# Performance work log

Hardware: AMD Instinct MI355X
Metric: run time of the kernel (lower is better)

## Reference

```python
import jax, jax.numpy as jnp
import numpy as np

B, S, E, H, L, F, V = 8, 1024, 768, 12, 6, 3072, 32000
HD = E // H  # head_dim = 64
EPS = 1e-5


def _pos_encoding(max_len, dim):
    pos = np.arange(max_len, dtype=np.float32)[:, None]
    div = np.exp(np.arange(0, dim, 2, dtype=np.float32) * (-np.log(10000.0) / dim))
    pe = np.zeros((max_len, dim), dtype=np.float32)
    pe[:, 0::2] = np.sin(pos * div)
    pe[:, 1::2] = np.cos(pos * div)
    return jnp.asarray(pe)


def setup_inputs() -> dict:
    key = jax.random.key(0)
    ks = jax.random.split(key, 16)
    sd = 0.02
    inp = {}
    inp['input_ids'] = jax.random.randint(ks[0], (B, S), 0, V)
    inp['attention_mask'] = jnp.ones((B, S), dtype=jnp.int32)
    inp['emb'] = jax.random.normal(ks[1], (V, E), jnp.float32) * sd
    inp['pe'] = _pos_encoding(S, E)
    inp['Wq'] = jax.random.normal(ks[2], (L, E, E), jnp.float32) * sd
    inp['bq'] = jnp.zeros((L, E), jnp.float32)
    inp['Wk'] = jax.random.normal(ks[3], (L, E, E), jnp.float32) * sd
    inp['bk'] = jnp.zeros((L, E), jnp.float32)
    inp['Wv'] = jax.random.normal(ks[4], (L, E, E), jnp.float32) * sd
    inp['bv'] = jnp.zeros((L, E), jnp.float32)
    inp['Wo'] = jax.random.normal(ks[5], (L, E, E), jnp.float32) * sd
    inp['bo'] = jnp.zeros((L, E), jnp.float32)
    inp['ln1_g'] = jnp.ones((L, E), jnp.float32)
    inp['ln1_b'] = jnp.zeros((L, E), jnp.float32)
    inp['W1'] = jax.random.normal(ks[6], (L, E, F), jnp.float32) * sd
    inp['b1'] = jnp.zeros((L, F), jnp.float32)
    inp['W2'] = jax.random.normal(ks[7], (L, F, E), jnp.float32) * sd
    inp['b2'] = jnp.zeros((L, E), jnp.float32)
    inp['ln2_g'] = jnp.ones((L, E), jnp.float32)
    inp['ln2_b'] = jnp.zeros((L, E), jnp.float32)
    inp['Wc'] = jax.random.normal(ks[8], (E, 2), jnp.float32) * sd
    inp['bc'] = jnp.zeros((2,), jnp.float32)
    return inp


def _layernorm(x, g, b):
    mu = jnp.mean(x, axis=-1, keepdims=True)
    var = jnp.mean(jnp.square(x - mu), axis=-1, keepdims=True)
    return (x - mu) * jax.lax.rsqrt(var + EPS) * g + b


def reference(input_ids, attention_mask, emb, pe, Wq, bq, Wk, bk, Wv, bv, Wo, bo,
              ln1_g, ln1_b, W1, b1, W2, b2, ln2_g, ln2_b, Wc, bc):
    x = emb[input_ids] + pe[None, :S, :]           # [B,S,E] (dropout = eval identity)
    mask = attention_mask[:, None, None, :]        # [B,1,1,S]
    scale = jnp.sqrt(jnp.float32(HD))

    def block(x, p):
        wq, bq_, wk, bk_, wv, bv_, wo, bo_, g1, be1, w1, b1_, w2, b2_, g2, be2 = p
        q = (x @ wq + bq_).reshape(B, S, H, HD).transpose(0, 2, 1, 3)  # [B,H,S,D]
        k = (x @ wk + bk_).reshape(B, S, H, HD).transpose(0, 2, 1, 3)
        v = (x @ wv + bv_).reshape(B, S, H, HD).transpose(0, 2, 1, 3)
        scores = jnp.einsum('bhsd,bhtd->bhst', q, k) / scale          # [B,H,S,S]
        scores = jnp.where(mask == 0, -jnp.inf, scores)
        attn = jax.nn.softmax(scores, axis=-1)
        o = jnp.einsum('bhst,bhtd->bhsd', attn, v)
        o = o.transpose(0, 2, 1, 3).reshape(B, S, E) @ wo + bo_
        x = _layernorm(x + o, g1, be1)
        ffn = jax.nn.relu(x @ w1 + b1_) @ w2 + b2_
        x = _layernorm(x + ffn, g2, be2)
        return x, None

    params = (Wq, bq, Wk, bk, Wv, bv, Wo, bo, ln1_g, ln1_b, W1, b1, W2, b2, ln2_g, ln2_b)
    x, _ = jax.lax.scan(block, x, params)
    pooled = jnp.mean(x, axis=1)                   # [B,E]
    return pooled @ Wc + bc                        # [B,2]
```

## Files before the change

kernel.cpp:

```cpp
#include <hip/hip_runtime.h>

typedef __bf16 bf16x8 __attribute__((ext_vector_type(8)));
typedef float  f32x4  __attribute__((ext_vector_type(4)));

constexpr int Bb = 8, Ss = 1024, Ee = 768, Hh = 12, Ll = 6, Ff = 3072;
constexpr int TOK  = Bb * Ss;
constexpr int NQKV = 3 * Ee;

static __device__ __forceinline__ f32x4 mfma16(bf16x8 a, bf16x8 b, f32x4 c) {
  return __builtin_amdgcn_mfma_f32_16x16x32_bf16(a, b, c, 0, 0, 0);
}

static __device__ __forceinline__ void async16(const void* g, void* l) {
  __builtin_amdgcn_global_load_lds(
      (const __attribute__((address_space(1))) unsigned int*)g,
      (__attribute__((address_space(3))) unsigned int*)l, 16, 0, 0);
}

static __device__ __forceinline__ bf16x8 ds_read128(const __bf16* p) {
  bf16x8 r;
  unsigned a = (unsigned)(size_t)p;
  asm volatile("ds_read_b128 %0, %1" : "=v"(r) : "v"(a));
  return r;
}

__global__ __launch_bounds__(256) void embed_kernel(
    const int* __restrict__ ids, const float* __restrict__ emb,
    const float* __restrict__ pe, float* __restrict__ x, __bf16* __restrict__ xb)
{
  int tok = blockIdx.x;
  int s   = tok & (Ss - 1);
  int id  = ids[tok];
  const float* er = emb + (size_t)id * Ee;
  const float* pr = pe  + (size_t)s  * Ee;
  size_t base = (size_t)tok * Ee;
#pragma unroll
  for (int i = 0; i < 3; i++) {
    int e = threadIdx.x + i * 256;
    float v = er[e] + pr[e];
    x[base + e]  = v;
    xb[base + e] = (__bf16)v;
  }
}

__global__ __launch_bounds__(256) void transpose_w_kernel(
    const float* __restrict__ src, __bf16* __restrict__ dst,
    int K, int N, size_t sls, size_t dls)
{
  __shared__ float t[32][33];
  src += (size_t)blockIdx.z * sls;
  dst += (size_t)blockIdx.z * dls;
  int n0 = blockIdx.x * 32, k0 = blockIdx.y * 32;
  int c = threadIdx.x & 31, r0 = threadIdx.x >> 5;
#pragma unroll
  for (int rr = 0; rr < 32; rr += 8)
    t[r0 + rr][c] = src[(size_t)(k0 + r0 + rr) * N + n0 + c];
  __syncthreads();
#pragma unroll
  for (int rr = 0; rr < 32; rr += 8)
    dst[(size_t)(n0 + r0 + rr) * K + k0 + c] = (__bf16)t[c][r0 + rr];
}

template<bool OUT_BF16, bool RELU>
__global__ __launch_bounds__(256, 3) void gemm_kernel(
    const __bf16* __restrict__ A, const __bf16* __restrict__ Bt,
    const float* __restrict__ bias0, const float* __restrict__ bias1,
    const float* __restrict__ bias2, int bseg,
    float* __restrict__ Cf, __bf16* __restrict__ Cb, int M, int N, int K)
{
  __shared__ __align__(16) __bf16 lA[3][64 * 64];
  __shared__ __align__(16) __bf16 lB[3][64 * 64];
  const int tid  = threadIdx.x;
  const int wave = tid >> 6, lane = tid & 63;
  const int quad = lane >> 4, c16 = lane & 15;
  const int wm = wave >> 1, wn = wave & 1;

  const int bid = blockIdx.x;
  const int xcd = bid & 7;
  const int lb  = bid >> 3;
  const int mb  = xcd * 8 + (lb & 7);
  const int nb  = lb >> 3;
  const size_t m0 = (size_t)mb * 128, n0 = (size_t)nb * 128;

  f32x4 acc[4][4] = {};

  const int s0l = tid >> 3;
  const int s0c = tid & 7;
  const int l0  = s0c ^ (s0l & 7);
  const int tr0 = (s0l << 1) | (l0 >> 2);
  const int gc0 = (l0 & 3) * 8;
  const int s1l = (tid + 256) >> 3;
  const int l1  = s0c ^ (s1l & 7);
  const int tr1 = (s1l << 1) | (l1 >> 2);
  const int gc1 = (l1 & 3) * 8;

  const __bf16* Ag0 = A  + (m0 + tr0) * K + gc0;
  const __bf16* Ag1 = A  + (m0 + tr1) * K + gc1;
  const __bf16* Bg0 = Bt + (n0 + tr0) * K + gc0;
  const __bf16* Bg1 = Bt + (n0 + tr1) * K + gc1;
  const int d0 = tid * 8;

  const int nk = K >> 5;

  auto stage = [&](int t, int slot) {
    const int kof = t << 5;
    async16(Ag0 + kof, &lA[slot][d0]);
    async16(Ag1 + kof, &lA[slot][d0 + 2048]);
    async16(Bg0 + kof, &lB[slot][d0]);
    async16(Bg1 + kof, &lB[slot][d0 + 2048]);
  };

  int aoff[4], boff[4];
#pragma unroll
  for (int f = 0; f < 4; f++) {
    int ra = wm * 64 + f * 16 + c16;
    int ja = ra >> 1;
    aoff[f] = ja * 64 + (((((ra & 1) << 2) | quad)) ^ (ja & 7)) * 8;
    int rb = wn * 64 + f * 16 + c16;
    int jb = rb >> 1;
    boff[f] = jb * 64 + (((((rb & 1) << 2) | quad)) ^ (jb & 7)) * 8;
  }

  stage(0, 0);
  stage(1, 1);
  asm volatile("s_waitcnt vmcnt(4)" ::: "memory");
  __builtin_amdgcn_s_barrier();
  __builtin_amdgcn_sched_barrier(0);

  int slot = 0;
  for (int t = 0; t < nk; ++t) {
    if (t + 2 < nk) {
      int ns = slot + 2; if (ns >= 3) ns -= 3;
      stage(t + 2, ns);
    }
    const __bf16* la = &lA[slot][0];
    const __bf16* lb = &lB[slot][0];
    bf16x8 af[4], bfr[4];
#pragma unroll
    for (int f = 0; f < 4; f++) af[f]  = ds_read128(la + aoff[f]);
#pragma unroll
    for (int f = 0; f < 4; f++) bfr[f] = ds_read128(lb + boff[f]);
    asm volatile("s_waitcnt lgkmcnt(0)" ::: "memory");
    __builtin_amdgcn_sched_barrier(0);
    __builtin_amdgcn_s_setprio(1);
#pragma unroll
    for (int mi = 0; mi < 4; mi++)
#pragma unroll
      for (int ni = 0; ni < 4; ni++)
        acc[mi][ni] = mfma16(af[mi], bfr[ni], acc[mi][ni]);
    __builtin_amdgcn_s_setprio(0);
    __builtin_amdgcn_sched_barrier(0);
    if (t + 2 < nk) asm volatile("s_waitcnt vmcnt(4)" ::: "memory");
    else            asm volatile("s_waitcnt vmcnt(0)" ::: "memory");
    __builtin_amdgcn_s_barrier();
    __builtin_amdgcn_sched_barrier(0);
    slot = (slot + 1 == 3) ? 0 : slot + 1;
  }

#pragma unroll
  for (int ni = 0; ni < 4; ni++) {
    int col = (int)n0 + wn * 64 + ni * 16 + c16;
    const float* bp = bias0;
    int cc = col;
    if (cc >= bseg) { bp = bias1; cc -= bseg; }
    if (cc >= bseg) { bp = bias2; cc -= bseg; }
    float bv = bp[cc];
#pragma unroll
    for (int mi = 0; mi < 4; mi++) {
#pragma unroll
      for (int rr = 0; rr < 4; rr++) {
        size_t row = m0 + wm * 64 + mi * 16 + quad * 4 + rr;
        float v = acc[mi][ni][rr] + bv;
        if (RELU) v = fmaxf(v, 0.f);
        if (OUT_BF16) Cb[row * N + col] = (__bf16)v;
        else          Cf[row * N + col] = v;
      }
    }
  }
}

__global__ __launch_bounds__(256) void vtrans_kernel(
    const __bf16* __restrict__ qkv, __bf16* __restrict__ vt)
{
  int tid  = blockIdx.x * 256 + threadIdx.x;
  int d    = tid & 63;
  int rest = tid >> 6;
  int sc   = rest & 127;
  int bh   = rest >> 7;
  int b = bh / Hh, h = bh % Hh;
  const __bf16* src = qkv + (size_t)(b * Ss + sc * 8) * NQKV + 2 * Ee + h * 64 + d;
  bf16x8 v;
#pragma unroll
  for (int i = 0; i < 8; i++) v[i] = src[(size_t)i * NQKV];
  *(bf16x8*)(vt + ((size_t)bh * 64 + d) * Ss + sc * 8) = v;
}

__global__ __launch_bounds__(512, 6) void attn_kernel(
    const __bf16* __restrict__ qkv, const __bf16* __restrict__ vt,
    const int* __restrict__ amask, __bf16* __restrict__ out)
{
  __shared__ __align__(16) __bf16 kbuf[2][64 * 64];
  __shared__ __align__(16) __bf16 vbuf[2][64 * 64];
  __shared__ __align__(16) __bf16 plds[8][16 * 68];
  const int idx = blockIdx.x;
  const int bh = idx % 96, qi = idx / 96;
  const int b = bh / Hh, h = bh % Hh;
  const int lane = threadIdx.x & 63, wave = threadIdx.x >> 6;
  const int quad = lane >> 4, c16 = lane & 15;
  const int q0 = qi * 128 + wave * 16;

  const __bf16* qbase = qkv + (size_t)(b * Ss + q0 + c16) * NQKV + h * 64 + quad * 8;
  bf16x8 qf0 = *(const bf16x8*)(qbase);
  bf16x8 qf1 = *(const bf16x8*)(qbase + 32);

  const int srow = threadIdx.x >> 3;
  const int scol = ((threadIdx.x & 7) ^ (srow & 7)) * 8;
  const __bf16* kg = qkv + (size_t)(b * Ss + srow) * NQKV + Ee + h * 64 + scol;
  const __bf16* vg = vt + ((size_t)bh * 64 + srow) * Ss + scol;

  const int sa8 = c16 & 7;
  const int rc0 = (quad ^ sa8) * 8;
  const int rc1 = ((quad + 4) ^ sa8) * 8;

  f32x4 o[4] = {};
  float lrow[4] = {0.f, 0.f, 0.f, 0.f};
  const int* mp = amask + b * Ss;
  __bf16* pw = &plds[wave][0];

  async16(kg, &kbuf[0][(size_t)threadIdx.x * 8]);
  async16(vg, &vbuf[0][(size_t)threadIdx.x * 8]);

  for (int t = 0; t < 16; t++) {
    const int tb = t * 64;
    __syncthreads();
    if (t < 15) {
      const int nb = (t + 1) & 1, ntb = tb + 64;
      async16(kg + (size_t)ntb * NQKV, &kbuf[nb][(size_t)threadIdx.x * 8]);
      async16(vg + ntb,                &vbuf[nb][(size_t)threadIdx.x * 8]);
    }
    const __bf16* kb = &kbuf[t & 1][0];
    const __bf16* vb = &vbuf[t & 1][0];

    f32x4 s[4];
#pragma unroll
    for (int n = 0; n < 4; n++) {
      bf16x8 kf0 = *(const bf16x8*)(kb + (n * 16 + c16) * 64 + rc0);
      bf16x8 kf1 = *(const bf16x8*)(kb + (n * 16 + c16) * 64 + rc1);
      f32x4 z = {};
      z = mfma16(qf0, kf0, z);
      s[n] = mfma16(qf1, kf1, z);
    }
    float mk[4];
#pragma unroll
    for (int n = 0; n < 4; n++) mk[n] = mp[tb + n * 16 + c16] ? 0.f : -1e30f;

#pragma unroll
    for (int rr = 0; rr < 4; rr++) {
      float p0 = __expf(s[0][rr] * 0.125f + mk[0]);
      float p1 = __expf(s[1][rr] * 0.125f + mk[1]);
      float p2 = __expf(s[2][rr] * 0.125f + mk[2]);
      float p3 = __expf(s[3][rr] * 0.125f + mk[3]);
      lrow[rr] += (p0 + p1) + (p2 + p3);
      int prow = (quad * 4 + rr) * 68;
      pw[prow + 0  + c16] = (__bf16)p0;
      pw[prow + 16 + c16] = (__bf16)p1;
      pw[prow + 32 + c16] = (__bf16)p2;
      pw[prow + 48 + c16] = (__bf16)p3;
    }

    bf16x8 pf0 = *(const bf16x8*)(pw + c16 * 68 + quad * 8);
    bf16x8 pf1 = *(const bf16x8*)(pw + c16 * 68 + 32 + quad * 8);
#pragma unroll
    for (int ni = 0; ni < 4; ni++) {
      bf16x8 vf0 = *(const bf16x8*)(vb + (ni * 16 + c16) * 64 + rc0);
      bf16x8 vf1 = *(const bf16x8*)(vb + (ni * 16 + c16) * 64 + rc1);
      o[ni] = mfma16(pf0, vf0, o[ni]);
      o[ni] = mfma16(pf1, vf1, o[ni]);
    }
  }

#pragma unroll
  for (int rr = 0; rr < 4; rr++) {
    float sr = lrow[rr];
    sr += __shfl_xor(sr, 1);
    sr += __shfl_xor(sr, 2);
    sr += __shfl_xor(sr, 4);
    sr += __shfl_xor(sr, 8);
    float inv = 1.f / sr;
    size_t row = (size_t)(b * Ss + q0 + quad * 4 + rr) * Ee + h * 64;
    out[row + 0  + c16] = (__bf16)(o[0][rr] * inv);
    out[row + 16 + c16] = (__bf16)(o[1][rr] * inv);
    out[row + 32 + c16] = (__bf16)(o[2][rr] * inv);
    out[row + 48 + c16] = (__bf16)(o[3][rr] * inv);
  }
}

__global__ __launch_bounds__(256) void add_ln_kernel(
    const float* __restrict__ xin, const float* __restrict__ tmp,
    const float* __restrict__ g, const float* __restrict__ beta,
    float* __restrict__ xout, __bf16* __restrict__ xbout)
{
  __shared__ float red[8];
  size_t base = (size_t)blockIdx.x * Ee;
  float hv[3], s = 0.f, sq = 0.f;
#pragma unroll
  for (int i = 0; i < 3; i++) {
    int e = threadIdx.x + i * 256;
    hv[i] = xin[base + e] + tmp[base + e];
    s += hv[i]; sq += hv[i] * hv[i];
  }
#pragma unroll
  for (int m = 1; m < 64; m <<= 1) { s += __shfl_xor(s, m); sq += __shfl_xor(sq, m); }
  int wave = threadIdx.x >> 6;
  if ((threadIdx.x & 63) == 0) { red[wave] = s; red[4 + wave] = sq; }
  __syncthreads();
  s  = red[0] + red[1] + red[2] + red[3];
  sq = red[4] + red[5] + red[6] + red[7];
  float mean = s * (1.f / Ee);
  float var  = sq * (1.f / Ee) - mean * mean;
  float rstd = rsqrtf(var + 1e-5f);
#pragma unroll
  for (int i = 0; i < 3; i++) {
    int e = threadIdx.x + i * 256;
    float v = (hv[i] - mean) * rstd * g[e] + beta[e];
    xout[base + e]  = v;
    xbout[base + e] = (__bf16)v;
  }
}

__global__ __launch_bounds__(256) void pool1_kernel(
    const float* __restrict__ x, float* __restrict__ partial)
{
  int b = blockIdx.x, chunk = blockIdx.y;
  float acc[3] = {0.f, 0.f, 0.f};
  for (int s = chunk * 64; s < chunk * 64 + 64; s++) {
#pragma unroll
    for (int i = 0; i < 3; i++) {
      int e = threadIdx.x + i * 256;
      acc[i] += x[((size_t)b * Ss + s) * Ee + e];
    }
  }
#pragma unroll
  for (int i = 0; i < 3; i++) {
    int e = threadIdx.x + i * 256;
    partial[((size_t)b * 16 + chunk) * Ee + e] = acc[i];
  }
}

__global__ __launch_bounds__(256) void pool2_kernel(
    const float* __restrict__ partial, const float* __restrict__ Wc,
    const float* __restrict__ bc, float* __restrict__ out)
{
  __shared__ float red[8];
  int b = blockIdx.x;
  float p0 = 0.f, p1 = 0.f;
#pragma unroll
  for (int i = 0; i < 3; i++) {
    int e = threadIdx.x + i * 256;
    float pe_ = 0.f;
#pragma unroll
    for (int c = 0; c < 16; c++) pe_ += partial[((size_t)b * 16 + c) * Ee + e];
    pe_ *= (1.f / Ss);
    p0 += pe_ * Wc[e * 2 + 0];
    p1 += pe_ * Wc[e * 2 + 1];
  }
#pragma unroll
  for (int m = 1; m < 64; m <<= 1) { p0 += __shfl_xor(p0, m); p1 += __shfl_xor(p1, m); }
  int wave = threadIdx.x >> 6;
  if ((threadIdx.x & 63) == 0) { red[wave] = p0; red[4 + wave] = p1; }
  __syncthreads();
  if (threadIdx.x == 0) {
    out[b * 2 + 0] = red[0] + red[1] + red[2] + red[3] + bc[0];
    out[b * 2 + 1] = red[4] + red[5] + red[6] + red[7] + bc[1];
  }
}

extern "C" void kernel_launch(void* const* d_in, const int* in_sizes, int n_in,
                              void* d_out, int out_size, void* d_ws, size_t ws_size,
                              hipStream_t stream) {
  const int*   ids   = (const int*)  d_in[0];
  const int*   amask = (const int*)  d_in[1];
  const float* emb   = (const float*)d_in[2];
  const float* pe    = (const float*)d_in[3];
  const float* Wq    = (const float*)d_in[4];
  const float* bq    = (const float*)d_in[5];
  const float* Wk    = (const float*)d_in[6];
  const float* bk    = (const float*)d_in[7];
  const float* Wv    = (const float*)d_in[8];
  const float* bv    = (const float*)d_in[9];
  const float* Wo    = (const float*)d_in[10];
  const float* bo    = (const float*)d_in[11];
  const float* ln1g  = (const float*)d_in[12];
  const float* ln1b  = (const float*)d_in[13];
  const float* W1    = (const float*)d_in[14];
  const float* b1    = (const float*)d_in[15];
  const float* W2    = (const float*)d_in[16];
  const float* b2    = (const float*)d_in[17];
  const float* ln2g  = (const float*)d_in[18];
  const float* ln2b  = (const float*)d_in[19];
  const float* Wc    = (const float*)d_in[20];
  const float* bc    = (const float*)d_in[21];
  float* outp = (float*)d_out;

  char* p = (char*)d_ws;
  auto alloc = [&](size_t bytes) { char* r = p; p += (bytes + 255) & ~(size_t)255; return r; };
  float*  x     = (float*) alloc((size_t)TOK * Ee * 4);
  __bf16* xb    = (__bf16*)alloc((size_t)TOK * Ee * 2);
  float*  tmp   = (float*) alloc((size_t)TOK * Ee * 4);
  __bf16* attn  = (__bf16*)alloc((size_t)TOK * Ee * 2);
  char*   r1    = alloc((size_t)TOK * Ff * 2);
  __bf16* qkv   = (__bf16*)r1;
  __bf16* vt    = (__bf16*)(r1 + (size_t)TOK * NQKV * 2);
  __bf16* h1    = (__bf16*)r1;
  __bf16* wqkvt = (__bf16*)alloc((size_t)Ll * NQKV * Ee * 2);
  __bf16* wot   = (__bf16*)alloc((size_t)Ll * Ee * Ee * 2);
  __bf16* w1t   = (__bf16*)alloc((size_t)Ll * Ff * Ee * 2);
  __bf16* w2t   = (__bf16*)alloc((size_t)Ll * Ee * Ff * 2);
  float*  part  = (float*) alloc((size_t)Bb * 16 * Ee * 4);

  embed_kernel<<<TOK, 256, 0, stream>>>(ids, emb, pe, x, xb);

  transpose_w_kernel<<<dim3(Ee/32, Ee/32, Ll), 256, 0, stream>>>(
      Wq, wqkvt,                         Ee, Ee, (size_t)Ee*Ee, (size_t)NQKV*Ee);
  transpose_w_kernel<<<dim3(Ee/32, Ee/32, Ll), 256, 0, stream>>>(
      Wk, wqkvt + (size_t)Ee*Ee,         Ee, Ee, (size_t)Ee*Ee, (size_t)NQKV*Ee);
  transpose_w_kernel<<<dim3(Ee/32, Ee/32, Ll), 256, 0, stream>>>(
      Wv, wqkvt + (size_t)2*Ee*Ee,       Ee, Ee, (size_t)Ee*Ee, (size_t)NQKV*Ee);
  transpose_w_kernel<<<dim3(Ee/32, Ee/32, Ll), 256, 0, stream>>>(
      Wo, wot,                           Ee, Ee, (size_t)Ee*Ee, (size_t)Ee*Ee);
  transpose_w_kernel<<<dim3(Ff/32, Ee/32, Ll), 256, 0, stream>>>(
      W1, w1t,                           Ee, Ff, (size_t)Ee*Ff, (size_t)Ff*Ee);
  transpose_w_kernel<<<dim3(Ee/32, Ff/32, Ll), 256, 0, stream>>>(
      W2, w2t,                           Ff, Ee, (size_t)Ff*Ee, (size_t)Ee*Ff);

  for (int l = 0; l < Ll; l++) {
    gemm_kernel<true, false><<<64 * (NQKV/128), 256, 0, stream>>>(
        xb, wqkvt + (size_t)l*NQKV*Ee,
        bq + l*Ee, bk + l*Ee, bv + l*Ee, Ee,
        nullptr, qkv, TOK, NQKV, Ee);
    vtrans_kernel<<<3072, 256, 0, stream>>>(qkv, vt);
    attn_kernel<<<768, 512, 0, stream>>>(qkv, vt, amask, attn);
    gemm_kernel<false, false><<<64 * (Ee/128), 256, 0, stream>>>(
        attn, wot + (size_t)l*Ee*Ee,
        bo + l*Ee, bo + l*Ee, bo + l*Ee, Ee,
        tmp, nullptr, TOK, Ee, Ee);
    add_ln_kernel<<<TOK, 256, 0, stream>>>(x, tmp, ln1g + l*Ee, ln1b + l*Ee, x, xb);
    gemm_kernel<true, true><<<64 * (Ff/128), 256, 0, stream>>>(
        xb, w1t + (size_t)l*Ff*Ee,
        b1 + l*Ff, b1 + l*Ff, b1 + l*Ff, Ff,
        nullptr, h1, TOK, Ff, Ee);
    gemm_kernel<false, false><<<64 * (Ee/128), 256, 0, stream>>>(
        h1, w2t + (size_t)l*Ee*Ff,
        b2 + l*Ee, b2 + l*Ee, b2 + l*Ee, Ee,
        tmp, nullptr, TOK, Ee, Ff);
    add_ln_kernel<<<TOK, 256, 0, stream>>>(x, tmp, ln2g + l*Ee, ln2b + l*Ee, x, xb);
  }

  pool1_kernel<<<dim3(Bb, 16), 256, 0, stream>>>(x, part);
  pool2_kernel<<<Bb, 256, 0, stream>>>(part, Wc, bc, outp);
}
```

Baseline: 1.910 ms.

## Add 256x128 triple-buffered GEMM for QKV/FFN1 and use exp2 in attention

```diff
diff --git a/kernel.cpp b/kernel.cpp
--- a/kernel.cpp
+++ b/kernel.cpp
@@ -22,6 +22,10 @@
   unsigned a = (unsigned)(size_t)p;
   asm volatile("ds_read_b128 %0, %1" : "=v"(r) : "v"(a));
   return r;
+}
+
+static __device__ __forceinline__ float fexp2(float x) {
+  float r; asm("v_exp_f32 %0, %1" : "=v"(r) : "v"(x)); return r;
 }
 
 __global__ __launch_bounds__(256) void embed_kernel(
@@ -179,6 +183,130 @@
   }
 }
 
+template<bool RELU>
+__global__ __launch_bounds__(256, 2) void gemm_big_kernel(
+    const __bf16* __restrict__ A, const __bf16* __restrict__ Bt,
+    const float* __restrict__ bias0, const float* __restrict__ bias1,
+    const float* __restrict__ bias2, int bseg,
+    __bf16* __restrict__ Cb, int N, int K)
+{
+  __shared__ __align__(16) __bf16 lA[3][128 * 64];
+  __shared__ __align__(16) __bf16 lB[3][64 * 64];
+  const int tid  = threadIdx.x;
+  const int wave = tid >> 6, lane = tid & 63;
+  const int quad = lane >> 4, c16 = lane & 15;
+  const int wm = wave >> 1, wn = wave & 1;
+
+  const int bid = blockIdx.x;
+  const int xcd = bid & 7;
+  const int lb  = bid >> 3;
+  const int mb  = xcd * 4 + (lb & 3);
+  const int nb  = lb >> 2;
+  const size_t m0 = (size_t)mb * 256, n0 = (size_t)nb * 128;
+
+  f32x4 acc[8][4] = {};
+
+  const __bf16* Agp[4];
+#pragma unroll
+  for (int j = 0; j < 4; j++) {
+    int s = tid + j * 256, lr = s >> 3, sc = s & 7;
+    int l = sc ^ (lr & 7);
+    int tr = (lr << 1) | (l >> 2), gc = (l & 3) * 8;
+    Agp[j] = A + (m0 + tr) * (size_t)K + gc;
+  }
+  const __bf16* Bgp[2];
+#pragma unroll
+  for (int j = 0; j < 2; j++) {
+    int s = tid + j * 256, lr = s >> 3, sc = s & 7;
+    int l = sc ^ (lr & 7);
+    int tr = (lr << 1) | (l >> 2), gc = (l & 3) * 8;
+    Bgp[j] = Bt + (n0 + tr) * (size_t)K + gc;
+  }
+  const int d0 = tid * 8;
+
+  const int nk = K >> 5;
+
+  auto stage = [&](int t, int slot) {
+    const int kof = t << 5;
+#pragma unroll
+    for (int j = 0; j < 4; j++)
+      async16(Agp[j] + kof, &lA[slot][d0 + j * 2048]);
+#pragma unroll
+    for (int j = 0; j < 2; j++)
+      async16(Bgp[j] + kof, &lB[slot][d0 + j * 2048]);
+  };
+
+  int aoff[8], boff[4];
+#pragma unroll
+  for (int f = 0; f < 8; f++) {
+    int ra = wm * 128 + f * 16 + c16;
+    int ja = ra >> 1;
+    aoff[f] = ja * 64 + ((((ra & 1) << 2) | quad) ^ (ja & 7)) * 8;
+  }
+#pragma unroll
+  for (int f = 0; f < 4; f++) {
+    int rb = wn * 64 + f * 16 + c16;
+    int jb = rb >> 1;
+    boff[f] = jb * 64 + ((((rb & 1) << 2) | quad) ^ (jb & 7)) * 8;
+  }
+
+  stage(0, 0);
+  stage(1, 1);
+  asm volatile("s_waitcnt vmcnt(6)" ::: "memory");
+  __builtin_amdgcn_s_barrier();
+  __builtin_amdgcn_sched_barrier(0);
+
+  int slot = 0;
+  for (int t = 0; t < nk; ++t) {
+    if (t + 2 < nk) {
+      int ns = slot + 2; if (ns >= 3) ns -= 3;
+      stage(t + 2, ns);
+    }
+    const __bf16* la  = &lA[slot][0];
+    const __bf16* lbp = &lB[slot][0];
+    bf16x8 af[8], bfr[4];
+#pragma unroll
+    for (int f = 0; f < 8; f++) af[f]  = ds_read128(la + aoff[f]);
+#pragma unroll
+    for (int f = 0; f < 4; f++) bfr[f] = ds_read128(lbp + boff[f]);
+    asm volatile("s_waitcnt lgkmcnt(0)" ::: "memory");
+    __builtin_amdgcn_sched_barrier(0);
+    __builtin_amdgcn_s_setprio(1);
+#pragma unroll
+    for (int mi = 0; mi < 8; mi++)
+#pragma unroll
+      for (int ni = 0; ni < 4; ni++)
+        acc[mi][ni] = mfma16(af[mi], bfr[ni], acc[mi][ni]);
+    __builtin_amdgcn_s_setprio(0);
+    __builtin_amdgcn_sched_barrier(0);
+    if (t + 2 < nk) asm volatile("s_waitcnt vmcnt(6)" ::: "memory");
+    else            asm volatile("s_waitcnt vmcnt(0)" ::: "memory");
+    __builtin_amdgcn_s_barrier();
+    __builtin_amdgcn_sched_barrier(0);
+    slot = (slot + 1 == 3) ? 0 : slot + 1;
+  }
+
+#pragma unroll
+  for (int ni = 0; ni < 4; ni++) {
+    int col = (int)n0 + wn * 64 + ni * 16 + c16;
+    const float* bp = bias0;
+    int cc = col;
+    if (cc >= bseg) { bp = bias1; cc -= bseg; }
+    if (cc >= bseg) { bp = bias2; cc -= bseg; }
+    float bv = bp[cc];
+#pragma unroll
+    for (int mi = 0; mi < 8; mi++) {
+#pragma unroll
+      for (int rr = 0; rr < 4; rr++) {
+        size_t row = m0 + wm * 128 + mi * 16 + quad * 4 + rr;
+        float v = acc[mi][ni][rr] + bv;
+        if (RELU) v = fmaxf(v, 0.f);
+        Cb[row * N + col] = (__bf16)v;
+      }
+    }
+  }
+}
+
 __global__ __launch_bounds__(256) void vtrans_kernel(
     const __bf16* __restrict__ qkv, __bf16* __restrict__ vt)
 {
@@ -226,6 +354,7 @@
   float lrow[4] = {0.f, 0.f, 0.f, 0.f};
   const int* mp = amask + b * Ss;
   __bf16* pw = &plds[wave][0];
+  const float CE = 0.18033688f;
 
   async16(kg, &kbuf[0][(size_t)threadIdx.x * 8]);
   async16(vg, &vbuf[0][(size_t)threadIdx.x * 8]);
@@ -241,25 +370,35 @@
     const __bf16* kb = &kbuf[t & 1][0];
     const __bf16* vb = &vbuf[t & 1][0];
 
+    float mk2[4];
+#pragma unroll
+    for (int n = 0; n < 4; n++) mk2[n] = mp[tb + n * 16 + c16] ? 0.f : -1e30f;
+    bf16x8 kf[8], vf[8];
+#pragma unroll
+    for (int n = 0; n < 4; n++) {
+      kf[2*n]   = *(const bf16x8*)(kb + (n * 16 + c16) * 64 + rc0);
+      kf[2*n+1] = *(const bf16x8*)(kb + (n * 16 + c16) * 64 + rc1);
+    }
+#pragma unroll
+    for (int n = 0; n < 4; n++) {
+      vf[2*n]   = *(const bf16x8*)(vb + (n * 16 + c16) * 64 + rc0);
+      vf[2*n+1] = *(const bf16x8*)(vb + (n * 16 + c16) * 64 + rc1);
+    }
+
     f32x4 s[4];
 #pragma unroll
     for (int n = 0; n < 4; n++) {
-      bf16x8 kf0 = *(const bf16x8*)(kb + (n * 16 + c16) * 64 + rc0);
-      bf16x8 kf1 = *(const bf16x8*)(kb + (n * 16 + c16) * 64 + rc1);
       f32x4 z = {};
-      z = mfma16(qf0, kf0, z);
-      s[n] = mfma16(qf1, kf1, z);
-    }
-    float mk[4];
-#pragma unroll
-    for (int n = 0; n < 4; n++) mk[n] = mp[tb + n * 16 + c16] ? 0.f : -1e30f;
+      z = mfma16(qf0, kf[2*n], z);
+      s[n] = mfma16(qf1, kf[2*n+1], z);
+    }
 
 #pragma unroll
     for (int rr = 0; rr < 4; rr++) {
-      float p0 = __expf(s[0][rr] * 0.125f + mk[0]);
-      float p1 = __expf(s[1][rr] * 0.125f + mk[1]);
-      float p2 = __expf(s[2][rr] * 0.125f + mk[2]);
-      float p3 = __expf(s[3][rr] * 0.125f + mk[3]);
+      float p0 = fexp2(fmaf(s[0][rr], CE, mk2[0]));
+      float p1 = fexp2(fmaf(s[1][rr], CE, mk2[1]));
+      float p2 = fexp2(fmaf(s[2][rr], CE, mk2[2]));
+      float p3 = fexp2(fmaf(s[3][rr], CE, mk2[3]));
       lrow[rr] += (p0 + p1) + (p2 + p3);
       int prow = (quad * 4 + rr) * 68;
       pw[prow + 0  + c16] = (__bf16)p0;
@@ -272,10 +411,8 @@
     bf16x8 pf1 = *(const bf16x8*)(pw + c16 * 68 + 32 + quad * 8);
 #pragma unroll
     for (int ni = 0; ni < 4; ni++) {
-      bf16x8 vf0 = *(const bf16x8*)(vb + (ni * 16 + c16) * 64 + rc0);
-      bf16x8 vf1 = *(const bf16x8*)(vb + (ni * 16 + c16) * 64 + rc1);
-      o[ni] = mfma16(pf0, vf0, o[ni]);
-      o[ni] = mfma16(pf1, vf1, o[ni]);
+      o[ni] = mfma16(pf0, vf[2*ni],   o[ni]);
+      o[ni] = mfma16(pf1, vf[2*ni+1], o[ni]);
     }
   }
 
@@ -434,10 +571,10 @@
       W2, w2t,                           Ff, Ee, (size_t)Ff*Ee, (size_t)Ee*Ff);
 
   for (int l = 0; l < Ll; l++) {
-    gemm_kernel<true, false><<<64 * (NQKV/128), 256, 0, stream>>>(
+    gemm_big_kernel<false><<<8 * 4 * (NQKV/128), 256, 0, stream>>>(
         xb, wqkvt + (size_t)l*NQKV*Ee,
         bq + l*Ee, bk + l*Ee, bv + l*Ee, Ee,
-        nullptr, qkv, TOK, NQKV, Ee);
+        qkv, NQKV, Ee);
     vtrans_kernel<<<3072, 256, 0, stream>>>(qkv, vt);
     attn_kernel<<<768, 512, 0, stream>>>(qkv, vt, amask, attn);
     gemm_kernel<false, false><<<64 * (Ee/128), 256, 0, stream>>>(
@@ -445,10 +582,10 @@
         bo + l*Ee, bo + l*Ee, bo + l*Ee, Ee,
         tmp, nullptr, TOK, Ee, Ee);
     add_ln_kernel<<<TOK, 256, 0, stream>>>(x, tmp, ln1g + l*Ee, ln1b + l*Ee, x, xb);
-    gemm_kernel<true, true><<<64 * (Ff/128), 256, 0, stream>>>(
+    gemm_big_kernel<true><<<8 * 4 * (Ff/128), 256, 0, stream>>>(
         xb, w1t + (size_t)l*Ff*Ee,
         b1 + l*Ff, b1 + l*Ff, b1 + l*Ff, Ff,
-        nullptr, h1, TOK, Ff, Ee);
+        h1, Ff, Ee);
     gemm_kernel<false, false><<<64 * (Ee/128), 256, 0, stream>>>(
         h1, w2t + (size_t)l*Ee*Ff,
         b2 + l*Ee, b2 + l*Ee, b2 + l*Ee, Ee,
```

Measured after the change: 1.928 ms. Within noise of the previous version (+0.9%).
